# Kernel optimization log

Hardware: AMD Instinct MI355X
Metric: run time of the kernel (lower is better)

The kernel has to match this reference:

```python
import jax, jax.numpy as jnp
import numpy as np

V = 2_000_000   # packed vertices
E = 6_000_000
C = 128         # in_channels
B = 64          # number of meshes in the batch


def setup_inputs() -> dict:
    key = jax.random.key(0)
    k1, k2, k3, k4, k5, k6, k7, k8 = jax.random.split(key, 8)
    verts = jax.random.normal(k1, (V, C), dtype=jnp.float32)
    edges = jax.random.randint(k2, (E, 2), 0, V, dtype=jnp.int64)
    verts_idx = jnp.sort(jax.random.randint(k3, (V,), 0, B, dtype=jnp.int64))
    edges_idx = jax.random.randint(k4, (E,), 0, B, dtype=jnp.int64)
    # GraphConv(in_channels, 1) params: w0 (self) and w1 (neighbor) Linear layers
    s = 1.0 / np.sqrt(C)
    w0 = jax.random.uniform(k5, (1, C), jnp.float32, -s, s)
    b0 = jax.random.uniform(k6, (1,), jnp.float32, -s, s)
    w1 = jax.random.uniform(k7, (1, C), jnp.float32, -s, s)
    b1 = jax.random.uniform(k8, (1,), jnp.float32, -s, s)
    return {"verts": verts, "edges": edges, "verts_idx": verts_idx,
            "edges_idx": edges_idx, "num_meshes": B,
            "w0": w0, "b0": b0, "w1": w1, "b1": b1}


def reference(verts, edges, verts_idx, edges_idx, num_meshes, w0, b0, w1, b1):
    # GraphConv: out_v = W0 x_v + b0 + sum_{u in N(v)} (W1 x_u + b1)
    h0 = verts @ w0.T + b0          # [V, 1] self term
    h1 = verts @ w1.T + b1          # [V, 1] neighbor term
    # undirected gather-scatter over the edge list (both directions)
    src, dst = edges[:, 0], edges[:, 1]
    nbr = jnp.zeros_like(h0)
    nbr = nbr.at[src].add(h1[dst])
    nbr = nbr.at[dst].add(h1[src])
    scores = jnp.tanh(h0 + nbr)     # [V, 1] per-vertex attention score
    # unpack by mesh id and take per-mesh max over vertices == segment max
    out = jax.ops.segment_max(scores[:, 0], verts_idx,
                              num_segments=num_meshes,
                              indices_are_sorted=True)
    return out.reshape(num_meshes, -1)   # [B, 1]
```

## Files before the change

kernel.cpp:

```cpp
#include <hip/hip_runtime.h>


constexpr int C = 128;

__device__ __forceinline__ unsigned int enc_f32(float f) {
    unsigned int b = __float_as_uint(f);
    return (b & 0x80000000u) ? ~b : (b | 0x80000000u);
}
__device__ __forceinline__ float dec_f32(unsigned int u) {
    unsigned int b = (u & 0x80000000u) ? (u ^ 0x80000000u) : ~u;
    return __uint_as_float(b);
}

__global__ void k_init(unsigned int* __restrict__ umax, int B) {
    int i = blockIdx.x * blockDim.x + threadIdx.x;
    if (i < B) umax[i] = enc_f32(-__builtin_huge_valf());
}

__global__ void k_diag(float* __restrict__ out, int B, float v) {
    int i = blockIdx.x * blockDim.x + threadIdx.x;
    if (i < B) out[i] = v;
}

__global__ void k_vertex(const float* __restrict__ verts,
                         const float* __restrict__ w0, const float* __restrict__ b0,
                         const float* __restrict__ w1, const float* __restrict__ b1,
                         float* __restrict__ acc, float* __restrict__ h1out,
                         int V) {
    int tid = blockIdx.x * blockDim.x + threadIdx.x;
    int sub = tid & 31;
    int v   = tid >> 5;
    if (v >= V) return;

    float4 wv0 = *reinterpret_cast<const float4*>(w0 + sub * 4);
    float4 wv1 = *reinterpret_cast<const float4*>(w1 + sub * 4);
    float4 x   = *reinterpret_cast<const float4*>(verts + (size_t)v * C + sub * 4);

    float d0 = x.x * wv0.x + x.y * wv0.y + x.z * wv0.z + x.w * wv0.w;
    float d1 = x.x * wv1.x + x.y * wv1.y + x.z * wv1.z + x.w * wv1.w;

    #pragma unroll
    for (int off = 16; off >= 1; off >>= 1) {
        d0 += __shfl_xor(d0, off, 32);
        d1 += __shfl_xor(d1, off, 32);
    }
    if (sub == 0) {
        acc[v]   = d0 + b0[0];
        h1out[v] = d1 + b1[0];
    }
}

__global__ void k_edge(const int* __restrict__ edges,
                       const float* __restrict__ h1,
                       float* __restrict__ acc, int E) {
    int e = blockIdx.x * blockDim.x + threadIdx.x;
    if (e >= E) return;
    int2 p = reinterpret_cast<const int2*>(edges)[e];
    int s = p.x, d = p.y;
    float hs = h1[s], hd = h1[d];
    atomicAdd(&acc[s], hd);
    atomicAdd(&acc[d], hs);
}

__global__ void k_pool(const float* __restrict__ acc,
                       const int* __restrict__ vidx,
                       unsigned int* __restrict__ umax, int V) {
    int v = blockIdx.x * blockDim.x + threadIdx.x;
    bool valid = v < V;
    int m = -1;
    unsigned int u = 0u;
    if (valid) {
        float s = tanhf(acc[v]);
        m = vidx[v];
        u = enc_f32(s);
    }
    int m0 = __shfl(m, 0);
    if (__all(m == m0)) {
        if (m0 >= 0) {
            #pragma unroll
            for (int off = 32; off >= 1; off >>= 1) {
                unsigned int o = __shfl_xor(u, off);
                u = (o > u) ? o : u;
            }
            if ((threadIdx.x & 63) == 0) atomicMax(&umax[m0], u);
        }
    } else {
        if (valid) atomicMax(&umax[m], u);
    }
}

__global__ void k_decode(const unsigned int* __restrict__ umax,
                         float* __restrict__ out, int B) {
    int i = blockIdx.x * blockDim.x + threadIdx.x;
    if (i < B) out[i] = dec_f32(umax[i]);
}

extern "C" void kernel_launch(void* const* d_in, const int* in_sizes, int n_in,
                              void* d_out, int out_size, void* d_ws, size_t ws_size,
                              hipStream_t stream) {
    const float* verts = (const float*)d_in[0];
    const int*   edges = (const int*)d_in[1];
    const int*   vidx  = (const int*)d_in[2];
    const float* w0 = (const float*)d_in[5];
    const float* b0 = (const float*)d_in[6];
    const float* w1 = (const float*)d_in[7];
    const float* b1 = (const float*)d_in[8];
    float* out = (float*)d_out;

    const int V = in_sizes[0] / C;
    const int E = in_sizes[1] / 2;
    const int B = out_size;

    const size_t need = (size_t)V * 4 * 2 + (size_t)B * 4;
    if (ws_size < need) {
        hipLaunchKernelGGL(k_diag, dim3(1), dim3(256), 0, stream,
                           out, B, (float)ws_size);
        return;
    }

    float* acc = (float*)d_ws;
    float* h1  = acc + V;
    unsigned int* umax = (unsigned int*)(h1 + V);

    hipLaunchKernelGGL(k_init, dim3(1), dim3(256), 0, stream, umax, B);

    {
        long long threads = (long long)V * 32;
        int block = 256;
        unsigned grid = (unsigned)((threads + block - 1) / block);
        hipLaunchKernelGGL(k_vertex, dim3(grid), dim3(block), 0, stream,
                           verts, w0, b0, w1, b1, acc, h1, V);
    }

    hipLaunchKernelGGL(k_edge, dim3((E + 255) / 256), dim3(256), 0, stream,
                       edges, h1, acc, E);

    hipLaunchKernelGGL(k_pool, dim3((V + 255) / 256), dim3(256), 0, stream,
                       acc, vidx, umax, V);

    hipLaunchKernelGGL(k_decode, dim3(1), dim3(256), 0, stream, umax, out, B);
}
```

Measured before the change: 1.031 ms.

## Widen per-thread work in vertex, edge and pool kernels with vector loads

```diff
diff --git a/kernel.cpp b/kernel.cpp
--- a/kernel.cpp
+++ b/kernel.cpp
@@ -2,6 +2,8 @@
 
 
 constexpr int C = 128;
+
+typedef float vfloat4 __attribute__((ext_vector_type(4)));
 
 __device__ __forceinline__ unsigned int enc_f32(float f) {
     unsigned int b = __float_as_uint(f);
@@ -22,27 +24,35 @@
     if (i < B) out[i] = v;
 }
 
-__global__ void k_vertex(const float* __restrict__ verts,
-                         const float* __restrict__ w0, const float* __restrict__ b0,
-                         const float* __restrict__ w1, const float* __restrict__ b1,
-                         float* __restrict__ acc, float* __restrict__ h1out,
-                         int V) {
+__global__ __launch_bounds__(256) void k_vertex(
+        const float* __restrict__ verts,
+        const float* __restrict__ w0, const float* __restrict__ b0,
+        const float* __restrict__ w1, const float* __restrict__ b1,
+        float* __restrict__ acc, float* __restrict__ h1out,
+        int V) {
     int tid = blockIdx.x * blockDim.x + threadIdx.x;
-    int sub = tid & 31;
-    int v   = tid >> 5;
+    int sub = tid & 15;
+    int v   = tid >> 4;
     if (v >= V) return;
 
-    float4 wv0 = *reinterpret_cast<const float4*>(w0 + sub * 4);
-    float4 wv1 = *reinterpret_cast<const float4*>(w1 + sub * 4);
-    float4 x   = *reinterpret_cast<const float4*>(verts + (size_t)v * C + sub * 4);
+    const vfloat4* row = reinterpret_cast<const vfloat4*>(verts + (size_t)v * C);
+    const vfloat4* W0  = reinterpret_cast<const vfloat4*>(w0);
+    const vfloat4* W1  = reinterpret_cast<const vfloat4*>(w1);
 
-    float d0 = x.x * wv0.x + x.y * wv0.y + x.z * wv0.z + x.w * wv0.w;
-    float d1 = x.x * wv1.x + x.y * wv1.y + x.z * wv1.z + x.w * wv1.w;
+    vfloat4 x0 = __builtin_nontemporal_load(&row[sub]);
+    vfloat4 x1 = __builtin_nontemporal_load(&row[sub + 16]);
+    vfloat4 a0 = W0[sub], a1 = W0[sub + 16];
+    vfloat4 c0 = W1[sub], c1 = W1[sub + 16];
+
+    float d0 = x0.x * a0.x + x0.y * a0.y + x0.z * a0.z + x0.w * a0.w
+             + x1.x * a1.x + x1.y * a1.y + x1.z * a1.z + x1.w * a1.w;
+    float d1 = x0.x * c0.x + x0.y * c0.y + x0.z * c0.z + x0.w * c0.w
+             + x1.x * c1.x + x1.y * c1.y + x1.z * c1.z + x1.w * c1.w;
 
     #pragma unroll
-    for (int off = 16; off >= 1; off >>= 1) {
-        d0 += __shfl_xor(d0, off, 32);
-        d1 += __shfl_xor(d1, off, 32);
+    for (int off = 8; off >= 1; off >>= 1) {
+        d0 += __shfl_xor(d0, off);
+        d1 += __shfl_xor(d1, off);
     }
     if (sub == 0) {
         acc[v]   = d0 + b0[0];
@@ -50,42 +60,70 @@
     }
 }
 
-__global__ void k_edge(const int* __restrict__ edges,
-                       const float* __restrict__ h1,
-                       float* __restrict__ acc, int E) {
-    int e = blockIdx.x * blockDim.x + threadIdx.x;
-    if (e >= E) return;
-    int2 p = reinterpret_cast<const int2*>(edges)[e];
-    int s = p.x, d = p.y;
-    float hs = h1[s], hd = h1[d];
-    atomicAdd(&acc[s], hd);
-    atomicAdd(&acc[d], hs);
+__global__ __launch_bounds__(256) void k_edge(
+        const int* __restrict__ edges,
+        const float* __restrict__ h1,
+        float* __restrict__ acc, int E) {
+    int t = blockIdx.x * blockDim.x + threadIdx.x;
+    int E2 = E >> 1;
+    if (t < E2) {
+        int4 p = reinterpret_cast<const int4*>(edges)[t];
+        float ha = h1[p.x], hb = h1[p.y], hc = h1[p.z], hd = h1[p.w];
+        atomicAdd(&acc[p.x], hb);
+        atomicAdd(&acc[p.y], ha);
+        atomicAdd(&acc[p.z], hd);
+        atomicAdd(&acc[p.w], hc);
+    } else if (t == E2 && (E & 1)) {
+        int s = edges[(size_t)(E - 1) * 2], d = edges[(size_t)(E - 1) * 2 + 1];
+        float hs = h1[s], hd = h1[d];
+        atomicAdd(&acc[s], hd);
+        atomicAdd(&acc[d], hs);
+    }
 }
 
-__global__ void k_pool(const float* __restrict__ acc,
-                       const int* __restrict__ vidx,
-                       unsigned int* __restrict__ umax, int V) {
-    int v = blockIdx.x * blockDim.x + threadIdx.x;
-    bool valid = v < V;
-    int m = -1;
-    unsigned int u = 0u;
+__global__ __launch_bounds__(256) void k_pool(
+        const float* __restrict__ acc,
+        const int* __restrict__ vidx,
+        unsigned int* __restrict__ umax, int V) {
+    int t = blockIdx.x * blockDim.x + threadIdx.x;
+    int V4 = V >> 2;
+    bool valid = t < V4;
+
+    int mlo = -1, mhi = -1;
+    unsigned int u0 = 0, u1 = 0, u2 = 0, u3 = 0;
     if (valid) {
-        float s = tanhf(acc[v]);
-        m = vidx[v];
-        u = enc_f32(s);
+        float4 a = reinterpret_cast<const float4*>(acc)[t];
+        int4   m = reinterpret_cast<const int4*>(vidx)[t];
+        u0 = enc_f32(tanhf(a.x)); u1 = enc_f32(tanhf(a.y));
+        u2 = enc_f32(tanhf(a.z)); u3 = enc_f32(tanhf(a.w));
+        mlo = m.x; mhi = m.w;
     }
-    int m0 = __shfl(m, 0);
-    if (__all(m == m0)) {
-        if (m0 >= 0) {
-            #pragma unroll
-            for (int off = 32; off >= 1; off >>= 1) {
-                unsigned int o = __shfl_xor(u, off);
-                u = (o > u) ? o : u;
-            }
-            if ((threadIdx.x & 63) == 0) atomicMax(&umax[m0], u);
+    unsigned int um = max(max(u0, u1), max(u2, u3));
+
+    int wlo = __shfl(mlo, 0);
+    int whi = __shfl(mhi, 63);
+    if (wlo == whi && __all(valid) && wlo >= 0) {
+        #pragma unroll
+        for (int off = 32; off >= 1; off >>= 1) {
+            unsigned int o = __shfl_xor(um, off);
+            um = (o > um) ? o : um;
         }
-    } else {
-        if (valid) atomicMax(&umax[m], u);
+        if ((threadIdx.x & 63) == 0) atomicMax(&umax[wlo], um);
+    } else if (valid) {
+        if (mlo == mhi) {
+            atomicMax(&umax[mlo], um);
+        } else {
+            int4 m = reinterpret_cast<const int4*>(vidx)[t];
+            atomicMax(&umax[m.x], u0);
+            atomicMax(&umax[m.y], u1);
+            atomicMax(&umax[m.z], u2);
+            atomicMax(&umax[m.w], u3);
+        }
+    }
+    int rem = V & 3;
+    if (t < rem) {
+        int v = V4 * 4 + t;
+        atomicMax(&umax[vidx[v]], enc_f32(tanhf(acc[v])));
     }
 }
 
@@ -122,21 +160,26 @@
     float* h1  = acc + V;
     unsigned int* umax = (unsigned int*)(h1 + V);
 
-    hipLaunchKernelGGL(k_init, dim3(1), dim3(256), 0, stream, umax, B);
+    hipLaunchKernelGGL(k_init, dim3(1), dim3(64), 0, stream, umax, B);
 
     {
-        long long threads = (long long)V * 32;
-        int block = 256;
-        unsigned grid = (unsigned)((threads + block - 1) / block);
-        hipLaunchKernelGGL(k_vertex, dim3(grid), dim3(block), 0, stream,
+        long long threads = (long long)V * 16;
+        unsigned grid = (unsigned)((threads + 255) / 256);
+        hipLaunchKernelGGL(k_vertex, dim3(grid), dim3(256), 0, stream,
                            verts, w0, b0, w1, b1, acc, h1, V);
     }
 
-    hipLaunchKernelGGL(k_edge, dim3((E + 255) / 256), dim3(256), 0, stream,
-                       edges, h1, acc, E);
+    {
+        int work = (E >> 1) + 1;
+        hipLaunchKernelGGL(k_edge, dim3((work + 255) / 256), dim3(256), 0, stream,
+                           edges, h1, acc, E);
+    }
 
-    hipLaunchKernelGGL(k_pool, dim3((V + 255) / 256), dim3(256), 0, stream,
-                       acc, vidx, umax, V);
+    {
+        int work = (V >> 2) + 4;
+        hipLaunchKernelGGL(k_pool, dim3((work + 255) / 256), dim3(256), 0, stream,
+                           acc, vidx, umax, V);
+    }
 
-    hipLaunchKernelGGL(k_decode, dim3(1), dim3(256), 0, stream, umax, out, B);
+    hipLaunchKernelGGL(k_decode, dim3(1), dim3(64), 0, stream, umax, out, B);
 }
```

After: 838.5 us. -18.7%, faster.
